# Optimization experiments

Hardware: AMD Instinct MI355X
Metric: run time of the kernel (lower is better)

## Reference

```python
import jax, jax.numpy as jnp
import numpy as np

B, S, D = 8, 2048, 512

def setup_inputs() -> dict:
    key = jax.random.key(0)
    k1, k2, k3, k4, k5 = jax.random.split(key, 5)
    scale_w = 1.0 / np.sqrt(D)
    return {
        "input_vector": jax.random.normal(k1, (B, S, D), dtype=jnp.float32),
        "mask": jax.random.randint(k2, (B, S), 0, 2, dtype=jnp.int32),
        "Wq": jax.random.normal(k3, (D, D), dtype=jnp.float32) * scale_w,
        "Wk": jax.random.normal(k4, (D, D), dtype=jnp.float32) * scale_w,
        "Wv": jax.random.normal(k5, (D, D), dtype=jnp.float32) * scale_w,
    }

def reference(input_vector, mask, Wq, Wk, Wv):
    # torch nn.Linear(bias=False): x @ W.T
    q = jnp.einsum('bsd,ed->bse', input_vector, Wq)
    k = jnp.einsum('bsd,ed->bse', input_vector, Wk)
    v = jnp.einsum('bsd,ed->bse', input_vector, Wv)
    # NOTE: original scales by sqrt(k.size(1)) == sqrt(seq_len), a quirk we preserve.
    scale = jnp.asarray(S, q.dtype) ** 0.5
    scores = jnp.einsum('bqd,bkd->bqk', q, k) / scale  # [B,S,S]
    m = mask[:, None, :]  # unsqueeze(1) -> broadcast over query dim
    scores = jnp.where(m == 0, -jnp.inf, scores)
    probs = jax.nn.softmax(scores, axis=-1)
    return jnp.einsum('bqk,bkd->bqd', probs, v)
```

## Files before the change

kernel.cpp:

```cpp
#include <hip/hip_runtime.h>
#include <cstdint>
#include <cstddef>

#define BB 8
#define SS 2048
#define DD 512

typedef __attribute__((ext_vector_type(8))) short bf16x8;
typedef __attribute__((ext_vector_type(4))) float f32x4;

__device__ __forceinline__ unsigned short f2bf(float f) {
  unsigned int u = __builtin_bit_cast(unsigned int, f);
  u = (u + 0x7FFFu + ((u >> 16) & 1u)) >> 16;
  return (unsigned short)u;
}
__device__ __forceinline__ float bf2f(unsigned short s) {
  return __builtin_bit_cast(float, ((unsigned int)s) << 16);
}

__device__ __forceinline__ void gload_lds16(const unsigned short* g, unsigned short* l) {
  __builtin_amdgcn_global_load_lds(
      (const __attribute__((address_space(1))) void*)g,
      (__attribute__((address_space(3))) void*)l, 16, 0, 0);
}

__device__ __forceinline__ void gemm_tile(
    const unsigned short* __restrict__ A,
    const unsigned short* __restrict__ B,
    int K, unsigned short* lA, unsigned short* lB,
    f32x4 acc[4][4], size_t m0, size_t n0)
{
  const int t = threadIdx.x;
  const int l = t & 63;
  const int w = t >> 6;
  const int wr = w >> 1, wc = w & 1;
  const size_t K64 = (size_t)K * 64;

  const unsigned short* gA = A + (m0 + (size_t)(t >> 2)) * (size_t)K + (size_t)((t & 3) * 8);
  const unsigned short* gB = B + (n0 + (size_t)(t >> 2)) * (size_t)K + (size_t)((t & 3) * 8);

  const int ar = (wr * 64 + (l & 15)) * 32 + (l >> 4) * 8;
  const int br = (wc * 64 + (l & 15)) * 32 + (l >> 4) * 8;

  const int nk = K >> 5;
  int buf = 0;

  gload_lds16(gA, lA + t * 8);
  gload_lds16(gA + K64, lA + 2048 + t * 8);
  gload_lds16(gB, lB + t * 8);
  gload_lds16(gB + K64, lB + 2048 + t * 8);

  for (int kt = 0; kt < nk; ++kt) {
    __syncthreads();
    if (kt + 1 < nk) {
      const int ko = (kt + 1) << 5;
      const int lo = (buf ^ 1) * 4096;
      gload_lds16(gA + ko, lA + lo + t * 8);
      gload_lds16(gA + ko + K64, lA + lo + 2048 + t * 8);
      gload_lds16(gB + ko, lB + lo + t * 8);
      gload_lds16(gB + ko + K64, lB + lo + 2048 + t * 8);
    }
    const unsigned short* pa = lA + buf * 4096 + ar;
    const unsigned short* pb = lB + buf * 4096 + br;
    bf16x8 af[4], bfr[4];
#pragma unroll
    for (int m = 0; m < 4; ++m) af[m] = *(const bf16x8*)(pa + m * 512);
#pragma unroll
    for (int n = 0; n < 4; ++n) bfr[n] = *(const bf16x8*)(pb + n * 512);
#pragma unroll
    for (int m = 0; m < 4; ++m)
#pragma unroll
      for (int n = 0; n < 4; ++n)
        acc[m][n] = __builtin_amdgcn_mfma_f32_16x16x32_bf16(af[m], bfr[n], acc[m][n], 0, 0, 0);
    buf ^= 1;
  }
}

__global__ __launch_bounds__(256) void convert_k(
    const float* __restrict__ X, const float* __restrict__ Wq,
    const float* __restrict__ Wk, const float* __restrict__ Wv,
    unsigned short* __restrict__ dst)
{
  const size_t NXe = (size_t)BB * SS * DD;
  const size_t NWe = (size_t)DD * DD;
  size_t i = ((size_t)blockIdx.x * 256 + threadIdx.x) * 4;
  const float* src;
  size_t off;
  if (i < NXe)                { src = X;  off = i; }
  else if (i < NXe + NWe)     { src = Wq; off = i - NXe; }
  else if (i < NXe + 2 * NWe) { src = Wk; off = i - NXe - NWe; }
  else                        { src = Wv; off = i - NXe - 2 * NWe; }
  float4 f = *(const float4*)(src + off);
  ushort4 o;
  o.x = f2bf(f.x); o.y = f2bf(f.y); o.z = f2bf(f.z); o.w = f2bf(f.w);
  *(ushort4*)(dst + i) = o;
}

__global__ __launch_bounds__(256, 2) void qkv_gemm_k(
    const unsigned short* __restrict__ Xb,
    const unsigned short* __restrict__ Wall,
    unsigned short* __restrict__ Qb,
    unsigned short* __restrict__ Kb,
    unsigned short* __restrict__ Vtb)
{
  __shared__ __align__(16) unsigned short lA[8192];
  __shared__ __align__(16) unsigned short lB[8192];
  const int z = blockIdx.z;
  const unsigned short* Bw = Wall + (size_t)z * (DD * DD);
  const size_t m0 = (size_t)blockIdx.y * 128;
  const size_t n0 = (size_t)blockIdx.x * 128;
  f32x4 acc[4][4];
#pragma unroll
  for (int m = 0; m < 4; ++m)
#pragma unroll
    for (int n = 0; n < 4; ++n) acc[m][n] = (f32x4){0.f, 0.f, 0.f, 0.f};

  gemm_tile(Xb, Bw, DD, lA, lB, acc, m0, n0);

  const int t = threadIdx.x, l = t & 63, w = t >> 6, wr = w >> 1, wc = w & 1;
  const size_t rb = m0 + (size_t)(wr * 64 + ((l >> 4) * 4));
  const int cb = (int)n0 + wc * 64 + (l & 15);
  if (z < 2) {
    unsigned short* O = z ? Kb : Qb;
    const float sc = z ? 1.0f : 0.022097086912079608f;
#pragma unroll
    for (int m = 0; m < 4; ++m)
#pragma unroll
      for (int n = 0; n < 4; ++n)
#pragma unroll
        for (int j = 0; j < 4; ++j) {
          size_t r = rb + (size_t)(m * 16 + j);
          O[r * DD + (size_t)(cb + n * 16)] = f2bf(acc[m][n][j] * sc);
        }
  } else {
#pragma unroll
    for (int m = 0; m < 4; ++m)
#pragma unroll
      for (int n = 0; n < 4; ++n)
#pragma unroll
        for (int j = 0; j < 4; ++j) {
          size_t r = rb + (size_t)(m * 16 + j);
          size_t bb = r >> 11, s = r & 2047;
          Vtb[((bb * DD + (size_t)(cb + n * 16)) << 11) + s] = f2bf(acc[m][n][j]);
        }
  }
}

__global__ __launch_bounds__(256, 2) void scores_gemm_k(
    const unsigned short* __restrict__ Qb,
    const unsigned short* __restrict__ Kb,
    unsigned short* __restrict__ Sc)
{
  __shared__ __align__(16) unsigned short lA[8192];
  __shared__ __align__(16) unsigned short lB[8192];
  const int lin = blockIdx.x;
  const int b = lin & 7;
  const int pos = lin >> 3;
  const int ty = pos & 15;
  const int tx = pos >> 4;
  const unsigned short* A  = Qb + (size_t)b * (SS * DD);
  const unsigned short* Bp = Kb + (size_t)b * (SS * DD);
  unsigned short* C = Sc + (size_t)b * ((size_t)SS * SS);
  const size_t m0 = (size_t)ty * 128;
  const size_t n0 = (size_t)tx * 128;
  f32x4 acc[4][4];
#pragma unroll
  for (int m = 0; m < 4; ++m)
#pragma unroll
    for (int n = 0; n < 4; ++n) acc[m][n] = (f32x4){0.f, 0.f, 0.f, 0.f};

  gemm_tile(A, Bp, DD, lA, lB, acc, m0, n0);

  const int t = threadIdx.x, l = t & 63, w = t >> 6, wr = w >> 1, wc = w & 1;
  const size_t rb = m0 + (size_t)(wr * 64 + ((l >> 4) * 4));
  const int cb = (int)n0 + wc * 64 + (l & 15);
#pragma unroll
  for (int m = 0; m < 4; ++m)
#pragma unroll
    for (int n = 0; n < 4; ++n)
#pragma unroll
      for (int j = 0; j < 4; ++j) {
        size_t r = rb + (size_t)(m * 16 + j);
        C[r * SS + (size_t)(cb + n * 16)] = f2bf(acc[m][n][j]);
      }
}

__global__ __launch_bounds__(256) void softmax_k(
    unsigned short* __restrict__ Sc, const int* __restrict__ mask)
{
  __shared__ float smax[4], ssum[4];
  const int row = blockIdx.x;
  const int b = row >> 11;
  unsigned short* p = Sc + (size_t)row * SS;
  const int* mk = mask + ((size_t)b << 11);
  const int t = threadIdx.x;
  const int c0 = t * 8;

  bf16x8 sv = *(const bf16x8*)(p + c0);
  int4 ma = *(const int4*)(mk + c0);
  int4 mb = *(const int4*)(mk + c0 + 4);
  int mm[8] = {ma.x, ma.y, ma.z, ma.w, mb.x, mb.y, mb.z, mb.w};
  float v[8];
#pragma unroll
  for (int j = 0; j < 8; ++j) v[j] = bf2f((unsigned short)sv[j]);

  float mx = -3.0e38f;
#pragma unroll
  for (int j = 0; j < 8; ++j) if (mm[j]) mx = fmaxf(mx, v[j]);
#pragma unroll
  for (int off = 32; off >= 1; off >>= 1) mx = fmaxf(mx, __shfl_xor(mx, off));
  const int wid = t >> 6, ln = t & 63;
  if (ln == 0) smax[wid] = mx;
  __syncthreads();
  mx = fmaxf(fmaxf(smax[0], smax[1]), fmaxf(smax[2], smax[3]));

  float e[8];
  float sum = 0.f;
#pragma unroll
  for (int j = 0; j < 8; ++j) { e[j] = mm[j] ? __expf(v[j] - mx) : 0.f; sum += e[j]; }
#pragma unroll
  for (int off = 32; off >= 1; off >>= 1) sum += __shfl_xor(sum, off);
  if (ln == 0) ssum[wid] = sum;
  __syncthreads();
  sum = ssum[0] + ssum[1] + ssum[2] + ssum[3];
  const float inv = 1.f / sum;

  bf16x8 ov;
#pragma unroll
  for (int j = 0; j < 8; ++j) ov[j] = (short)f2bf(e[j] * inv);
  *(bf16x8*)(p + c0) = ov;
}

__global__ __launch_bounds__(256, 2) void pv_gemm_k(
    const unsigned short* __restrict__ Sc,
    const unsigned short* __restrict__ Vtb,
    float* __restrict__ Out)
{
  __shared__ __align__(16) unsigned short lA[8192];
  __shared__ __align__(16) unsigned short lB[8192];
  const int lin = blockIdx.x;
  const int b = lin & 7;
  const int pos = lin >> 3;
  const int tx = pos & 3;
  const int ty = pos >> 2;
  const unsigned short* A  = Sc + (size_t)b * ((size_t)SS * SS);
  const unsigned short* Bp = Vtb + (size_t)b * (DD * SS);
  float* C = Out + (size_t)b * (SS * DD);
  const size_t m0 = (size_t)ty * 128;
  const size_t n0 = (size_t)tx * 128;
  f32x4 acc[4][4];
#pragma unroll
  for (int m = 0; m < 4; ++m)
#pragma unroll
    for (int n = 0; n < 4; ++n) acc[m][n] = (f32x4){0.f, 0.f, 0.f, 0.f};

  gemm_tile(A, Bp, SS, lA, lB, acc, m0, n0);

  const int t = threadIdx.x, l = t & 63, w = t >> 6, wr = w >> 1, wc = w & 1;
  const size_t rb = m0 + (size_t)(wr * 64 + ((l >> 4) * 4));
  const int cb = (int)n0 + wc * 64 + (l & 15);
#pragma unroll
  for (int m = 0; m < 4; ++m)
#pragma unroll
    for (int n = 0; n < 4; ++n)
#pragma unroll
      for (int j = 0; j < 4; ++j) {
        size_t r = rb + (size_t)(m * 16 + j);
        C[r * DD + (size_t)(cb + n * 16)] = acc[m][n][j];
      }
}

extern "C" void kernel_launch(void* const* d_in, const int* in_sizes, int n_in,
                              void* d_out, int out_size, void* d_ws, size_t ws_size,
                              hipStream_t stream) {
  const float* X    = (const float*)d_in[0];
  const int*   mask = (const int*)d_in[1];
  const float* Wq   = (const float*)d_in[2];
  const float* Wk   = (const float*)d_in[3];
  const float* Wv   = (const float*)d_in[4];

  unsigned short* ws   = (unsigned short*)d_ws;
  unsigned short* Xb   = ws;
  unsigned short* Wall = ws + 8388608;
  unsigned short* Qb   = ws + 9175040;
  unsigned short* Kb   = ws + 17563648;
  unsigned short* Vtb  = ws + 25952256;
  unsigned short* Sc   = ws + 34340864;
  float* Out = (float*)d_out;

  convert_k<<<8960, 256, 0, stream>>>(X, Wq, Wk, Wv, ws);

  qkv_gemm_k<<<dim3(4, 128, 3), 256, 0, stream>>>(Xb, Wall, Qb, Kb, Vtb);

  scores_gemm_k<<<2048, 256, 0, stream>>>(Qb, Kb, Sc);

  softmax_k<<<16384, 256, 0, stream>>>(Sc, mask);

  pv_gemm_k<<<512, 256, 0, stream>>>(Sc, Vtb, Out);
}
```

Baseline: 254.7 us.

## Use BK=64 XOR-swizzled LDS tiles and LDS-staged coalesced bf16 epilogue stores

The shared GEMM tile now loads a 64-wide K slice per stage instead of 32, with an XOR swizzle on the LDS column slot. This halves the number of barriers per tile and is meant to avoid LDS bank conflicts on fragment reads. The bf16 epilogues for Q/K, the transposed V and the scores matrix are staged through LDS and then written with 16-byte coalesced stores, replacing scattered 2-byte stores. The convert kernel now handles 8 elements per thread. In exchange, LDS use doubles to 64KB per block, which may limit occupancy.

```diff
diff --git a/kernel.cpp b/kernel.cpp
--- a/kernel.cpp
+++ b/kernel.cpp
@@ -24,7 +24,7 @@
       (__attribute__((address_space(3))) void*)l, 16, 0, 0);
 }
 
-__device__ __forceinline__ void gemm_tile(
+__device__ __forceinline__ void gemm_tile64(
     const unsigned short* __restrict__ A,
     const unsigned short* __restrict__ B,
     int K, unsigned short* lA, unsigned short* lB,
@@ -34,46 +34,84 @@
   const int l = t & 63;
   const int w = t >> 6;
   const int wr = w >> 1, wc = w & 1;
-  const size_t K64 = (size_t)K * 64;
-
-  const unsigned short* gA = A + (m0 + (size_t)(t >> 2)) * (size_t)K + (size_t)((t & 3) * 8);
-  const unsigned short* gB = B + (n0 + (size_t)(t >> 2)) * (size_t)K + (size_t)((t & 3) * 8);
-
-  const int ar = (wr * 64 + (l & 15)) * 32 + (l >> 4) * 8;
-  const int br = (wc * 64 + (l & 15)) * 32 + (l >> 4) * 8;
-
-  const int nk = K >> 5;
+
+  const int srow = t >> 3;
+  const int scol = ((t & 7) ^ (srow & 7)) * 8;
+  const unsigned short* gA = A + (m0 + (size_t)srow) * (size_t)K + scol;
+  const unsigned short* gB = B + (n0 + (size_t)srow) * (size_t)K + scol;
+  const size_t K32 = (size_t)K * 32;
+
+  const int nk = K >> 6;
   int buf = 0;
 
-  gload_lds16(gA, lA + t * 8);
-  gload_lds16(gA + K64, lA + 2048 + t * 8);
-  gload_lds16(gB, lB + t * 8);
-  gload_lds16(gB + K64, lB + 2048 + t * 8);
+#pragma unroll
+  for (int r = 0; r < 4; ++r) {
+    gload_lds16(gA + (size_t)r * K32, lA + r * 2048 + t * 8);
+    gload_lds16(gB + (size_t)r * K32, lB + r * 2048 + t * 8);
+  }
 
   for (int kt = 0; kt < nk; ++kt) {
     __syncthreads();
     if (kt + 1 < nk) {
-      const int ko = (kt + 1) << 5;
-      const int lo = (buf ^ 1) * 4096;
-      gload_lds16(gA + ko, lA + lo + t * 8);
-      gload_lds16(gA + ko + K64, lA + lo + 2048 + t * 8);
-      gload_lds16(gB + ko, lB + lo + t * 8);
-      gload_lds16(gB + ko + K64, lB + lo + 2048 + t * 8);
+      const int ko = (kt + 1) << 6;
+      const int lo = (buf ^ 1) * 8192;
+#pragma unroll
+      for (int r = 0; r < 4; ++r) {
+        gload_lds16(gA + ko + (size_t)r * K32, lA + lo + r * 2048 + t * 8);
+        gload_lds16(gB + ko + (size_t)r * K32, lB + lo + r * 2048 + t * 8);
+      }
     }
-    const unsigned short* pa = lA + buf * 4096 + ar;
-    const unsigned short* pb = lB + buf * 4096 + br;
-    bf16x8 af[4], bfr[4];
-#pragma unroll
-    for (int m = 0; m < 4; ++m) af[m] = *(const bf16x8*)(pa + m * 512);
-#pragma unroll
-    for (int n = 0; n < 4; ++n) bfr[n] = *(const bf16x8*)(pb + n * 512);
-#pragma unroll
-    for (int m = 0; m < 4; ++m)
-#pragma unroll
-      for (int n = 0; n < 4; ++n)
-        acc[m][n] = __builtin_amdgcn_mfma_f32_16x16x32_bf16(af[m], bfr[n], acc[m][n], 0, 0, 0);
+    const unsigned short* pa = lA + buf * 8192;
+    const unsigned short* pb = lB + buf * 8192;
+#pragma unroll
+    for (int kk = 0; kk < 2; ++kk) {
+      bf16x8 af[4], bfr[4];
+#pragma unroll
+      for (int m = 0; m < 4; ++m) {
+        int row = wr * 64 + m * 16 + (l & 15);
+        int slot = (kk * 4 + (l >> 4)) ^ (l & 7);
+        af[m] = *(const bf16x8*)(pa + row * 64 + slot * 8);
+      }
+#pragma unroll
+      for (int n = 0; n < 4; ++n) {
+        int row = wc * 64 + n * 16 + (l & 15);
+        int slot = (kk * 4 + (l >> 4)) ^ (l & 7);
+        bfr[n] = *(const bf16x8*)(pb + row * 64 + slot * 8);
+      }
+#pragma unroll
+      for (int m = 0; m < 4; ++m)
+#pragma unroll
+        for (int n = 0; n < 4; ++n)
+          acc[m][n] = __builtin_amdgcn_mfma_f32_16x16x32_bf16(af[m], bfr[n], acc[m][n], 0, 0, 0);
+    }
     buf ^= 1;
   }
+}
+
+__device__ __forceinline__ void store_bf16_tile(
+    f32x4 acc[4][4], unsigned short* lds,
+    unsigned short* __restrict__ Ct, size_t ldc, float scl)
+{
+  const int t = threadIdx.x, l = t & 63, w = t >> 6;
+  const int wr = w >> 1, wc = w & 1;
+  __syncthreads();
+#pragma unroll
+  for (int m = 0; m < 4; ++m)
+#pragma unroll
+    for (int n = 0; n < 4; ++n)
+#pragma unroll
+      for (int j = 0; j < 4; ++j) {
+        int row = wr * 64 + m * 16 + (l >> 4) * 4 + j;
+        int col = wc * 64 + n * 16 + (l & 15);
+        lds[row * 136 + col] = f2bf(acc[m][n][j] * scl);
+      }
+  __syncthreads();
+  const int row = t >> 1;
+  const int c0 = (t & 1) * 64;
+#pragma unroll
+  for (int i = 0; i < 8; ++i)
+    *(bf16x8*)(Ct + (size_t)row * ldc + c0 + i * 8) =
+        *(const bf16x8*)(lds + row * 136 + c0 + i * 8);
 }
 
 __global__ __launch_bounds__(256) void convert_k(
@@ -83,17 +121,21 @@
 {
   const size_t NXe = (size_t)BB * SS * DD;
   const size_t NWe = (size_t)DD * DD;
-  size_t i = ((size_t)blockIdx.x * 256 + threadIdx.x) * 4;
+  size_t i = ((size_t)blockIdx.x * 256 + threadIdx.x) * 8;
   const float* src;
   size_t off;
   if (i < NXe)                { src = X;  off = i; }
   else if (i < NXe + NWe)     { src = Wq; off = i - NXe; }
   else if (i < NXe + 2 * NWe) { src = Wk; off = i - NXe - NWe; }
   else                        { src = Wv; off = i - NXe - 2 * NWe; }
-  float4 f = *(const float4*)(src + off);
-  ushort4 o;
-  o.x = f2bf(f.x); o.y = f2bf(f.y); o.z = f2bf(f.z); o.w = f2bf(f.w);
-  *(ushort4*)(dst + i) = o;
+  float4 f0 = *(const float4*)(src + off);
+  float4 f1 = *(const float4*)(src + off + 4);
+  bf16x8 o;
+  o[0] = (short)f2bf(f0.x); o[1] = (short)f2bf(f0.y);
+  o[2] = (short)f2bf(f0.z); o[3] = (short)f2bf(f0.w);
+  o[4] = (short)f2bf(f1.x); o[5] = (short)f2bf(f1.y);
+  o[6] = (short)f2bf(f1.z); o[7] = (short)f2bf(f1.w);
+  *(bf16x8*)(dst + i) = o;
 }
 
 __global__ __launch_bounds__(256, 2) void qkv_gemm_k(
@@ -103,8 +145,7 @@
     unsigned short* __restrict__ Kb,
     unsigned short* __restrict__ Vtb)
 {
-  __shared__ __align__(16) unsigned short lA[8192];
-  __shared__ __align__(16) unsigned short lB[8192];
+  __shared__ __align__(16) unsigned short sh[32768];
   const int z = blockIdx.z;
   const unsigned short* Bw = Wall + (size_t)z * (DD * DD);
   const size_t m0 = (size_t)blockIdx.y * 128;
@@ -115,34 +156,34 @@
 #pragma unroll
     for (int n = 0; n < 4; ++n) acc[m][n] = (f32x4){0.f, 0.f, 0.f, 0.f};
 
-  gemm_tile(Xb, Bw, DD, lA, lB, acc, m0, n0);
+  gemm_tile64(Xb, Bw, DD, sh, sh + 16384, acc, m0, n0);
 
   const int t = threadIdx.x, l = t & 63, w = t >> 6, wr = w >> 1, wc = w & 1;
-  const size_t rb = m0 + (size_t)(wr * 64 + ((l >> 4) * 4));
-  const int cb = (int)n0 + wc * 64 + (l & 15);
   if (z < 2) {
     unsigned short* O = z ? Kb : Qb;
     const float sc = z ? 1.0f : 0.022097086912079608f;
+    store_bf16_tile(acc, sh, O + m0 * DD + n0, DD, sc);
+  } else {
+    __syncthreads();
 #pragma unroll
     for (int m = 0; m < 4; ++m)
 #pragma unroll
       for (int n = 0; n < 4; ++n)
 #pragma unroll
         for (int j = 0; j < 4; ++j) {
-          size_t r = rb + (size_t)(m * 16 + j);
-          O[r * DD + (size_t)(cb + n * 16)] = f2bf(acc[m][n][j] * sc);
+          int row = wr * 64 + m * 16 + (l >> 4) * 4 + j;
+          int col = wc * 64 + n * 16 + (l & 15);
+          sh[col * 136 + row] = f2bf(acc[m][n][j]);
         }
-  } else {
-#pragma unroll
-    for (int m = 0; m < 4; ++m)
-#pragma unroll
-      for (int n = 0; n < 4; ++n)
-#pragma unroll
-        for (int j = 0; j < 4; ++j) {
-          size_t r = rb + (size_t)(m * 16 + j);
-          size_t bb = r >> 11, s = r & 2047;
-          Vtb[((bb * DD + (size_t)(cb + n * 16)) << 11) + s] = f2bf(acc[m][n][j]);
-        }
+    __syncthreads();
+    const size_t bb = m0 >> 11;
+    const size_t sBase = m0 & 2047;
+    const int d = t >> 1;
+    const int s0 = (t & 1) * 64;
+    unsigned short* Vg = Vtb + (((bb * DD) + n0 + (size_t)d) << 11) + sBase;
+#pragma unroll
+    for (int i = 0; i < 8; ++i)
+      *(bf16x8*)(Vg + s0 + i * 8) = *(const bf16x8*)(sh + d * 136 + s0 + i * 8);
   }
 }
 
@@ -151,8 +192,7 @@
     const unsigned short* __restrict__ Kb,
     unsigned short* __restrict__ Sc)
 {
-  __shared__ __align__(16) unsigned short lA[8192];
-  __shared__ __align__(16) unsigned short lB[8192];
+  __shared__ __align__(16) unsigned short sh[32768];
   const int lin = blockIdx.x;
   const int b = lin & 7;
   const int pos = lin >> 3;
@@ -169,20 +209,9 @@
 #pragma unroll
     for (int n = 0; n < 4; ++n) acc[m][n] = (f32x4){0.f, 0.f, 0.f, 0.f};
 
-  gemm_tile(A, Bp, DD, lA, lB, acc, m0, n0);
-
-  const int t = threadIdx.x, l = t & 63, w = t >> 6, wr = w >> 1, wc = w & 1;
-  const size_t rb = m0 + (size_t)(wr * 64 + ((l >> 4) * 4));
-  const int cb = (int)n0 + wc * 64 + (l & 15);
-#pragma unroll
-  for (int m = 0; m < 4; ++m)
-#pragma unroll
-    for (int n = 0; n < 4; ++n)
-#pragma unroll
-      for (int j = 0; j < 4; ++j) {
-        size_t r = rb + (size_t)(m * 16 + j);
-        C[r * SS + (size_t)(cb + n * 16)] = f2bf(acc[m][n][j]);
-      }
+  gemm_tile64(A, Bp, DD, sh, sh + 16384, acc, m0, n0);
+
+  store_bf16_tile(acc, sh, C + m0 * SS + n0, SS, 1.0f);
 }
 
 __global__ __launch_bounds__(256) void softmax_k(
@@ -236,8 +265,7 @@
     const unsigned short* __restrict__ Vtb,
     float* __restrict__ Out)
 {
-  __shared__ __align__(16) unsigned short lA[8192];
-  __shared__ __align__(16) unsigned short lB[8192];
+  __shared__ __align__(16) unsigned short sh[32768];
   const int lin = blockIdx.x;
   const int b = lin & 7;
   const int pos = lin >> 3;
@@ -254,7 +282,7 @@
 #pragma unroll
     for (int n = 0; n < 4; ++n) acc[m][n] = (f32x4){0.f, 0.f, 0.f, 0.f};
 
-  gemm_tile(A, Bp, SS, lA, lB, acc, m0, n0);
+  gemm_tile64(A, Bp, SS, sh, sh + 16384, acc, m0, n0);
 
   const int t = threadIdx.x, l = t & 63, w = t >> 6, wr = w >> 1, wc = w & 1;
   const size_t rb = m0 + (size_t)(wr * 64 + ((l >> 4) * 4));
@@ -288,7 +316,7 @@
   unsigned short* Sc   = ws + 34340864;
   float* Out = (float*)d_out;
 
-  convert_k<<<8960, 256, 0, stream>>>(X, Wq, Wk, Wv, ws);
+  convert_k<<<4480, 256, 0, stream>>>(X, Wq, Wk, Wv, ws);
 
   qkv_gemm_k<<<dim3(4, 128, 3), 256, 0, stream>>>(Xb, Wall, Qb, Kb, Vtb);
 
```

Result: no change. 257.6 us (+1.1%).
